# Performance work log

Hardware: AMD Instinct MI355X
Metric: run time of the kernel (lower is better)

## Reference

```python
import jax, jax.numpy as jnp
import numpy as np
import math

B, S, E = 2, 2048, 1024
NH, NKV, HD = 16, 4, 64
GATE_CH = 12

def _rope(x, cos, sin):
    h = x.shape[-1] // 2
    x1, x2 = x[..., :h], x[..., h:]
    return jnp.concatenate((x1 * cos + x2 * sin, x1 * -sin + x2 * cos), axis=-1)

def _rms_norm(x):
    eps = jnp.finfo(x.dtype).eps
    return x * jax.lax.rsqrt(jnp.mean(x * x, axis=-1, keepdims=True) + eps)

def setup_inputs() -> dict:
    key = jax.random.key(0)
    ks = jax.random.split(key, 9)
    x = jax.random.normal(ks[0], (B, S, E), dtype=jnp.float32)
    ve = jax.random.normal(ks[1], (B, S, NKV * HD), dtype=jnp.float32)
    t = jnp.arange(S, dtype=jnp.float32)[:, None]
    inv_freq = 1.0 / (10000.0 ** (jnp.arange(0, HD // 2, dtype=jnp.float32) / (HD // 2)))
    ang = t * inv_freq[None, :]
    cos = jnp.cos(ang)[None, :, None, :]  # (1,S,1,HD//2)
    sin = jnp.sin(ang)[None, :, None, :]
    attn_mask = jnp.tril(jnp.ones((S, S), dtype=bool))[None, None]  # causal (1,1,S,S)
    sc = 0.02
    Wq = jax.random.normal(ks[2], (NH * HD, E), dtype=jnp.float32) * sc
    Wk = jax.random.normal(ks[3], (NKV * HD, E), dtype=jnp.float32) * sc
    Wv = jax.random.normal(ks[4], (NKV * HD, E), dtype=jnp.float32) * sc
    Wproj = jax.random.normal(ks[5], (E, E), dtype=jnp.float32) * sc
    Wgate = jax.random.normal(ks[6], (NKV, GATE_CH), dtype=jnp.float32) * sc
    return {"x": x, "ve": ve, "cos": cos, "sin": sin, "attn_mask": attn_mask,
            "Wq": Wq, "Wk": Wk, "Wv": Wv, "Wproj": Wproj, "Wgate": Wgate}

def reference(x, ve, cos, sin, attn_mask, Wq, Wk, Wv, Wproj, Wgate):
    b, s, _ = x.shape
    q = (x @ Wq.T).reshape(b, s, NH, HD)
    k = (x @ Wk.T).reshape(b, s, NKV, HD)
    v = (x @ Wv.T).reshape(b, s, NKV, HD)
    # value-embedding gating
    gate = 3.0 * jax.nn.sigmoid(x[..., :GATE_CH] @ Wgate.T)  # (b,s,NKV)
    v = v + gate[..., None] * ve.reshape(b, s, NKV, HD)
    # RoPE + QK-RMSNorm
    q = _rms_norm(_rope(q, cos, sin)) * 1.2
    k = _rms_norm(_rope(k, cos, sin)) * 1.2
    # GQA: repeat KV heads
    rep = NH // NKV
    k = jnp.repeat(k, rep, axis=2)
    v = jnp.repeat(v, rep, axis=2)
    q = q.transpose(0, 2, 1, 3)  # (b,h,s,d)
    k = k.transpose(0, 2, 1, 3)
    v = v.transpose(0, 2, 1, 3)
    scores = jnp.einsum('bhqd,bhkd->bhqk', q, k) / math.sqrt(HD)
    scores = jnp.where(attn_mask, scores, jnp.finfo(scores.dtype).min)
    attn = jax.nn.softmax(scores, axis=-1)
    y = jnp.einsum('bhqk,bhkd->bhqd', attn, v)
    y = y.transpose(0, 2, 1, 3).reshape(b, s, NH * HD)
    return y @ Wproj.T
```

## Files before the change

### kernel.cpp

```cpp
#include <hip/hip_runtime.h>
#include <hip/hip_bf16.h>
#include <math.h>

typedef short bf16x8 __attribute__((ext_vector_type(8)));
typedef float f32x4 __attribute__((ext_vector_type(4)));

#define LROW 72

__device__ __forceinline__ unsigned short f2bf(float f) {
  union { float f; unsigned int u; } v; v.f = f;
  unsigned int u = v.u;
  unsigned int r = (u + 0x7fffu + ((u >> 16) & 1u)) >> 16;
  return (unsigned short)r;
}
__device__ __forceinline__ float bf2f(unsigned short u) {
  return __uint_as_float((unsigned)u << 16);
}

#if __has_builtin(__builtin_amdgcn_global_load_lds)
#define HAVE_GLD 1
__device__ __forceinline__ void gld16(const void* g, void* l) {
  __builtin_amdgcn_global_load_lds(
      (const __attribute__((address_space(1))) unsigned int*)g,
      (__attribute__((address_space(3))) unsigned int*)l, 16, 0, 0);
}
#else
#define HAVE_GLD 0
#endif

__global__ __launch_bounds__(256) void cvt_all_kernel(const float* __restrict__ x,
                                                      const float* __restrict__ Wq,
                                                      const float* __restrict__ Wk,
                                                      const float* __restrict__ Wv,
                                                      const float* __restrict__ Wproj,
                                                      unsigned short* __restrict__ xb,
                                                      unsigned short* __restrict__ wqkv,
                                                      unsigned short* __restrict__ wpj) {
  int blk = blockIdx.x;
  const float* src;
  unsigned short* dst;
  if (blk < 4096)      { src = x + (size_t)blk * 1024;            dst = xb + (size_t)blk * 1024; }
  else if (blk < 5120) { src = Wq + (size_t)(blk - 4096) * 1024;  dst = wqkv + (size_t)(blk - 4096) * 1024; }
  else if (blk < 5376) { src = Wk + (size_t)(blk - 5120) * 1024;  dst = wqkv + (size_t)(blk - 4096) * 1024; }
  else if (blk < 5632) { src = Wv + (size_t)(blk - 5376) * 1024;  dst = wqkv + (size_t)(blk - 4096) * 1024; }
  else                 { src = Wproj + (size_t)(blk - 5632) * 1024; dst = wpj + (size_t)(blk - 5632) * 1024; }
  int i = threadIdx.x;
  float4 v = ((const float4*)src)[i];
  ushort4 o;
  o.x = f2bf(v.x); o.y = f2bf(v.y); o.z = f2bf(v.z); o.w = f2bf(v.w);
  ((ushort4*)dst)[i] = o;
}

__global__ __launch_bounds__(256) void gemm128_kernel(const unsigned short* __restrict__ A,
                                                      const unsigned short* __restrict__ B,
                                                      float* __restrict__ C, int M, int N, int K) {
  __shared__ unsigned short As[128 * 64];
  __shared__ unsigned short Bs[128 * 64];
  int tid = threadIdx.x;
  int wave = tid >> 6, lane = tid & 63, l15 = lane & 15, quad = lane >> 4;
  int wm = (wave >> 1) * 64, wn = (wave & 1) * 64;
  int n0 = blockIdx.x * 128, m0 = blockIdx.y * 128;
  f32x4 acc[4][4];
#pragma unroll
  for (int i = 0; i < 4; i++)
#pragma unroll
    for (int j = 0; j < 4; j++) acc[i][j] = (f32x4){0.f, 0.f, 0.f, 0.f};
  int srow = lane >> 3;
  int scol = ((lane & 7) ^ srow) * 8;
  for (int k0 = 0; k0 < K; k0 += 64) {
    __syncthreads();
#if HAVE_GLD
#pragma unroll
    for (int i = 0; i < 4; i++) {
      int row = wave * 32 + i * 8;
      gld16(A + (size_t)(m0 + row + srow) * K + k0 + scol, As + row * 64 + lane * 8);
      gld16(B + (size_t)(n0 + row + srow) * K + k0 + scol, Bs + row * 64 + lane * 8);
    }
#else
#pragma unroll
    for (int i = 0; i < 4; i++) {
      int row = wave * 32 + i * 8;
      *(float4*)(As + row * 64 + lane * 8) = *(const float4*)(A + (size_t)(m0 + row + srow) * K + k0 + scol);
      *(float4*)(Bs + row * 64 + lane * 8) = *(const float4*)(B + (size_t)(n0 + row + srow) * K + k0 + scol);
    }
#endif
    __syncthreads();
#pragma unroll
    for (int s = 0; s < 2; s++) {
      bf16x8 af[4], bf[4];
#pragma unroll
      for (int i = 0; i < 4; i++)
        af[i] = *(const bf16x8*)(As + (wm + i * 16 + l15) * 64 + (((s * 4 + quad) ^ (l15 & 7)) * 8));
#pragma unroll
      for (int j = 0; j < 4; j++)
        bf[j] = *(const bf16x8*)(Bs + (wn + j * 16 + l15) * 64 + (((s * 4 + quad) ^ (l15 & 7)) * 8));
#pragma unroll
      for (int i = 0; i < 4; i++)
#pragma unroll
        for (int j = 0; j < 4; j++)
          acc[i][j] = __builtin_amdgcn_mfma_f32_16x16x32_bf16(af[i], bf[j], acc[i][j], 0, 0, 0);
    }
  }
#pragma unroll
  for (int i = 0; i < 4; i++)
#pragma unroll
    for (int j = 0; j < 4; j++)
#pragma unroll
      for (int r = 0; r < 4; r++)
        C[(size_t)(m0 + wm + i * 16 + quad * 4 + r) * N + n0 + wn + j * 16 + l15] = acc[i][j][r];
}

__global__ __launch_bounds__(256) void gemm_qkv_kernel(const unsigned short* __restrict__ A,
                                                       const unsigned short* __restrict__ B,
                                                       const float* __restrict__ ve,
                                                       const float* __restrict__ cosb,
                                                       const float* __restrict__ sinb,
                                                       const float* __restrict__ wgate,
                                                       unsigned short* __restrict__ Q,
                                                       unsigned short* __restrict__ Kd,
                                                       unsigned short* __restrict__ Vt) {
  __shared__ unsigned short As[128 * 64];
  __shared__ unsigned short Bs[128 * 64];
  __shared__ float gLDS[256];
  const int K = 1024;
  int tid = threadIdx.x;
  int wave = tid >> 6, lane = tid & 63, l15 = lane & 15, quad = lane >> 4;
  int wm = (wave >> 1) * 64, wn = (wave & 1) * 64;
  int n0 = blockIdx.x * 128, m0 = blockIdx.y * 128;
  if (n0 >= 1280) {
    int rl = tid & 127, khl2 = tid >> 7;
    int kh = ((n0 >> 6) - 20) + khl2;
    float dot = 0.f;
#pragma unroll
    for (int jj = 0; jj < 12; jj++)
      dot += bf2f(A[(size_t)(m0 + rl) * 1024 + jj]) * wgate[kh * 12 + jj];
    gLDS[khl2 * 128 + rl] = 3.0f / (1.0f + __expf(-dot));
  }
  f32x4 acc[4][4];
#pragma unroll
  for (int i = 0; i < 4; i++)
#pragma unroll
    for (int j = 0; j < 4; j++) acc[i][j] = (f32x4){0.f, 0.f, 0.f, 0.f};
  int srow = lane >> 3;
  int scol = ((lane & 7) ^ srow) * 8;
  for (int k0 = 0; k0 < K; k0 += 64) {
    __syncthreads();
#if HAVE_GLD
#pragma unroll
    for (int i = 0; i < 4; i++) {
      int row = wave * 32 + i * 8;
      gld16(A + (size_t)(m0 + row + srow) * K + k0 + scol, As + row * 64 + lane * 8);
      gld16(B + (size_t)(n0 + row + srow) * K + k0 + scol, Bs + row * 64 + lane * 8);
    }
#else
#pragma unroll
    for (int i = 0; i < 4; i++) {
      int row = wave * 32 + i * 8;
      *(float4*)(As + row * 64 + lane * 8) = *(const float4*)(A + (size_t)(m0 + row + srow) * K + k0 + scol);
      *(float4*)(Bs + row * 64 + lane * 8) = *(const float4*)(B + (size_t)(n0 + row + srow) * K + k0 + scol);
    }
#endif
    __syncthreads();
#pragma unroll
    for (int s = 0; s < 2; s++) {
      bf16x8 af[4], bf[4];
#pragma unroll
      for (int i = 0; i < 4; i++)
        af[i] = *(const bf16x8*)(As + (wm + i * 16 + l15) * 64 + (((s * 4 + quad) ^ (l15 & 7)) * 8));
#pragma unroll
      for (int j = 0; j < 4; j++)
        bf[j] = *(const bf16x8*)(Bs + (wn + j * 16 + l15) * 64 + (((s * 4 + quad) ^ (l15 & 7)) * 8));
#pragma unroll
      for (int i = 0; i < 4; i++)
#pragma unroll
        for (int j = 0; j < 4; j++)
          acc[i][j] = __builtin_amdgcn_mfma_f32_16x16x32_bf16(af[i], bf[j], acc[i][j], 0, 0, 0);
    }
  }
  int hs = (n0 + wn) >> 6;
  if (hs < 20) {
    bool isq = hs < 16;
    float postscale = isq ? 0.216404256f : 1.2f;
#pragma unroll
    for (int i = 0; i < 4; i++) {
#pragma unroll
      for (int r = 0; r < 4; r++) {
        int row = m0 + wm + i * 16 + quad * 4 + r;
        int s = row & 2047, b = row >> 11;
        float c0 = cosb[s * 32 + l15],      s0 = sinb[s * 32 + l15];
        float c1 = cosb[s * 32 + 16 + l15], s1 = sinb[s * 32 + 16 + l15];
        float v0 = acc[i][0][r], v1 = acc[i][1][r], v2 = acc[i][2][r], v3 = acc[i][3][r];
        float n0v = fmaf(v0, c0,  v2 * s0);
        float n1v = fmaf(v1, c1,  v3 * s1);
        float n2v = fmaf(v2, c0, -v0 * s0);
        float n3v = fmaf(v3, c1, -v1 * s1);
        float ss = (n0v * n0v + n1v * n1v) + (n2v * n2v + n3v * n3v);
        ss += __shfl_xor(ss, 1, 64); ss += __shfl_xor(ss, 2, 64);
        ss += __shfl_xor(ss, 4, 64); ss += __shfl_xor(ss, 8, 64);
        float sc = rsqrtf(ss * (1.0f / 64.0f) + 1.1920929e-07f) * postscale;
        unsigned short* dp = isq ? Q + ((size_t)(b * 16 + hs) * 2048 + s) * 64
                                 : Kd + ((size_t)(b * 4 + hs - 16) * 2048 + s) * 64;
        dp[l15]      = f2bf(n0v * sc);
        dp[16 + l15] = f2bf(n1v * sc);
        dp[32 + l15] = f2bf(n2v * sc);
        dp[48 + l15] = f2bf(n3v * sc);
      }
    }
  } else {
    int khl = wave & 1;
    int kh = hs - 20;
#pragma unroll
    for (int i = 0; i < 4; i++) {
#pragma unroll
      for (int r = 0; r < 4; r++) {
        int rl = wm + i * 16 + quad * 4 + r;
        int row = m0 + rl, s = row & 2047, b = row >> 11;
        float g = gLDS[khl * 128 + rl];
        const float* vep = ve + (size_t)row * 256 + kh * 64;
        unsigned short* vp = Vt + ((size_t)(b * 4 + kh) * 64) * 2048 + s;
#pragma unroll
        for (int j = 0; j < 4; j++) {
          float vv = fmaf(g, vep[j * 16 + l15], acc[i][j][r]);
          vp[(size_t)(j * 16 + l15) * 2048] = f2bf(vv);
        }
      }
    }
  }
}

__global__ __launch_bounds__(256) void flash_kernel(const unsigned short* __restrict__ Q,
                                                    const unsigned short* __restrict__ K,
                                                    const unsigned short* __restrict__ Vt,
                                                    unsigned short* __restrict__ accP,
                                                    float* __restrict__ lP) {
  __shared__ unsigned short Ks[64 * LROW];
  __shared__ unsigned short Vs[64 * LROW];
  __shared__ unsigned short Ps[4 * 16 * LROW];
  int pair = blockIdx.x, h = blockIdx.y, bc = blockIdx.z;
  int b = bc >> 2, c = bc & 3;
  int hb = b * 16 + h;
  int kh = h >> 2;
  int tid = threadIdx.x, wave = tid >> 6, lane = tid & 63, l15 = lane & 15, quad = lane >> 4;
  const unsigned short* Kg = K + (size_t)(b * 4 + kh) * 2048 * 64;
  const unsigned short* Vg = Vt + (size_t)(b * 4 + kh) * 64 * 2048;
  unsigned short* Pw = Ps + wave * 16 * LROW;
  int row0 = tid >> 3, col8 = (tid & 7) * 8;

#pragma unroll
  for (int half = 0; half < 2; half++) {
    int qt = (half == 0) ? pair : 31 - pair;
    int c0t = ((qt + 1) * c) >> 2;
    int c1t = ((qt + 1) * (c + 1)) >> 2;
    int q0 = qt * 64;
    const unsigned short* Qp = Q + (((size_t)hb * 2048) + q0 + wave * 16 + l15) * 64;
    bf16x8 qf0 = *(const bf16x8*)(Qp + quad * 8);
    bf16x8 qf1 = *(const bf16x8*)(Qp + 32 + quad * 8);
    f32x4 acc[4];
#pragma unroll
    for (int i = 0; i < 4; i++) acc[i] = (f32x4){0.f, 0.f, 0.f, 0.f};
    float l_lane = 0.f;

    if (c1t > c0t) {
      int kf = c0t * 64;
      float4 pk0 = *(const float4*)(Kg + (size_t)(kf + row0) * 64 + col8);
      float4 pk1 = *(const float4*)(Kg + (size_t)(kf + row0 + 32) * 64 + col8);
      float4 pv0 = *(const float4*)(Vg + (size_t)row0 * 2048 + kf + col8);
      float4 pv1 = *(const float4*)(Vg + (size_t)(row0 + 32) * 2048 + kf + col8);

      for (int kt = c0t; kt < c1t; kt++) {
        int k0 = kt * 64;
        __syncthreads();
        *(float4*)(Ks + row0 * LROW + col8) = pk0;
        *(float4*)(Ks + (row0 + 32) * LROW + col8) = pk1;
        *(float4*)(Vs + row0 * LROW + col8) = pv0;
        *(float4*)(Vs + (row0 + 32) * LROW + col8) = pv1;
        if (kt + 1 < c1t) {
          int kn = k0 + 64;
          pk0 = *(const float4*)(Kg + (size_t)(kn + row0) * 64 + col8);
          pk1 = *(const float4*)(Kg + (size_t)(kn + row0 + 32) * 64 + col8);
          pv0 = *(const float4*)(Vg + (size_t)row0 * 2048 + kn + col8);
          pv1 = *(const float4*)(Vg + (size_t)(row0 + 32) * 2048 + kn + col8);
        }
        __syncthreads();

        f32x4 sv[4];
#pragma unroll
        for (int mt = 0; mt < 4; mt++) {
          sv[mt] = (f32x4){0.f, 0.f, 0.f, 0.f};
          bf16x8 k0f = *(const bf16x8*)(Ks + (mt * 16 + l15) * LROW + quad * 8);
          sv[mt] = __builtin_amdgcn_mfma_f32_16x16x32_bf16(k0f, qf0, sv[mt], 0, 0, 0);
          bf16x8 k1f = *(const bf16x8*)(Ks + (mt * 16 + l15) * LROW + 32 + quad * 8);
          sv[mt] = __builtin_amdgcn_mfma_f32_16x16x32_bf16(k1f, qf1, sv[mt], 0, 0, 0);
        }
        if (kt == qt) {
          int qg = q0 + wave * 16 + l15;
#pragma unroll
          for (int mt = 0; mt < 4; mt++) {
            int kg = k0 + mt * 16 + quad * 4;
#pragma unroll
            for (int r = 0; r < 4; r++)
              if (kg + r > qg) sv[mt][r] = -1e30f;
          }
        }
#pragma unroll
        for (int mt = 0; mt < 4; mt++) {
          float p0 = __builtin_amdgcn_exp2f(sv[mt][0]);
          float p1 = __builtin_amdgcn_exp2f(sv[mt][1]);
          float p2 = __builtin_amdgcn_exp2f(sv[mt][2]);
          float p3 = __builtin_amdgcn_exp2f(sv[mt][3]);
          l_lane += (p0 + p1) + (p2 + p3);
          unsigned int lo = __builtin_amdgcn_perm(__float_as_uint(p1), __float_as_uint(p0), 0x07060302u);
          unsigned int hi = __builtin_amdgcn_perm(__float_as_uint(p3), __float_as_uint(p2), 0x07060302u);
          *(uint2*)(Pw + l15 * LROW + mt * 16 + quad * 4) = make_uint2(lo, hi);
        }
#pragma unroll
        for (int step = 0; step < 2; step++) {
          bf16x8 pa = *(const bf16x8*)(Pw + l15 * LROW + step * 32 + quad * 8);
#pragma unroll
          for (int nt = 0; nt < 4; nt++) {
            bf16x8 vb = *(const bf16x8*)(Vs + (nt * 16 + l15) * LROW + step * 32 + quad * 8);
            acc[nt] = __builtin_amdgcn_mfma_f32_16x16x32_bf16(pa, vb, acc[nt], 0, 0, 0);
          }
        }
      }
    }
    l_lane += __shfl_xor(l_lane, 16, 64);
    l_lane += __shfl_xor(l_lane, 32, 64);

    size_t slot = (size_t)(c * 32 + hb) * 2048 + q0 + wave * 16;
    if (lane < 16) lP[slot + l15] = l_lane;
    unsigned short* aP = accP + slot * 64;
#pragma unroll
    for (int r = 0; r < 4; r++)
#pragma unroll
      for (int nt = 0; nt < 4; nt++)
        aP[(size_t)(quad * 4 + r) * 64 + nt * 16 + l15] = f2bf(acc[nt][r]);
  }
}

__global__ __launch_bounds__(256) void merge_kernel(const unsigned short* __restrict__ accP,
                                                    const float* __restrict__ lP,
                                                    unsigned short* __restrict__ Y) {
  int t = blockIdx.x * 256 + threadIdx.x;
  int d4 = (t & 15) * 4;
  int q  = (t >> 4) & 2047;
  int hb = t >> 15;
  const size_t CSTR = (size_t)32 * 2048 * 64;
  size_t pi = ((size_t)hb * 2048 + q) * 64 + d4;
  float y0 = 0.f, y1 = 0.f, y2 = 0.f, y3 = 0.f, l = 0.f;
#pragma unroll
  for (int c = 0; c < 4; c++) {
    ushort4 a = *(const ushort4*)(accP + pi + c * CSTR);
    y0 += bf2f(a.x); y1 += bf2f(a.y); y2 += bf2f(a.z); y3 += bf2f(a.w);
    l += lP[c * 65536 + hb * 2048 + q];
  }
  float inv = 1.f / l;
  ushort4 o;
  o.x = f2bf(y0 * inv); o.y = f2bf(y1 * inv); o.z = f2bf(y2 * inv); o.w = f2bf(y3 * inv);
  int b = hb >> 4, hh = hb & 15;
  *(ushort4*)(Y + ((size_t)(b * 2048 + q) * 1024) + hh * 64 + d4) = o;
}

extern "C" void kernel_launch(void* const* d_in, const int* in_sizes, int n_in,
                              void* d_out, int out_size, void* d_ws, size_t ws_size,
                              hipStream_t stream) {
  const float* x     = (const float*)d_in[0];
  const float* ve    = (const float*)d_in[1];
  const float* cosb  = (const float*)d_in[2];
  const float* sinb  = (const float*)d_in[3];
  const float* Wq    = (const float*)d_in[5];
  const float* Wk    = (const float*)d_in[6];
  const float* Wv    = (const float*)d_in[7];
  const float* Wproj = (const float*)d_in[8];
  const float* Wgate = (const float*)d_in[9];
  float* out = (float*)d_out;
  char* ws = (char*)d_ws;

  size_t o = 0;
  unsigned short* xb   = (unsigned short*)(ws + o); o += (size_t)4096 * 1024 * 2;
  unsigned short* wqkv = (unsigned short*)(ws + o); o += (size_t)1536 * 1024 * 2;
  unsigned short* wpj  = (unsigned short*)(ws + o); o += (size_t)1024 * 1024 * 2;
  unsigned short* Qb   = (unsigned short*)(ws + o); o += (size_t)2 * 16 * 2048 * 64 * 2;
  unsigned short* Kb   = (unsigned short*)(ws + o); o += (size_t)2 * 4 * 2048 * 64 * 2;
  unsigned short* Vb   = (unsigned short*)(ws + o); o += (size_t)2 * 4 * 2048 * 64 * 2;
  unsigned short* Yb   = (unsigned short*)(ws + o); o += (size_t)4096 * 1024 * 2;
  unsigned short* accP = (unsigned short*)(ws + o); o += (size_t)4 * 32 * 2048 * 64 * 2;
  float*          lP   = (float*)(ws + o);          o += (size_t)4 * 32 * 2048 * 4;

  hipLaunchKernelGGL(cvt_all_kernel, dim3(6656), dim3(256), 0, stream,
                     x, Wq, Wk, Wv, Wproj, xb, wqkv, wpj);
  hipLaunchKernelGGL(gemm_qkv_kernel, dim3(12, 32), dim3(256), 0, stream,
                     xb, wqkv, ve, cosb, sinb, Wgate, Qb, Kb, Vb);
  hipLaunchKernelGGL(flash_kernel, dim3(16, 16, 8), dim3(256), 0, stream, Qb, Kb, Vb, accP, lP);
  hipLaunchKernelGGL(merge_kernel, dim3(4096), dim3(256), 0, stream, accP, lP, Yb);
  hipLaunchKernelGGL(gemm128_kernel, dim3(8, 32), dim3(256), 0, stream, Yb, wpj, out, 4096, 1024, 1024);
}
```

Before: 200.3 us.

## Share KV tiles across GQA heads in flash kernel with double-buffered async loads

Each flash block now handles all four query heads that share one KV head, so every K/V tile loaded into LDS is reused four times. The grid drops from 16 heads to 4 KV heads, and the split-K factor rises from 4 to 6 to keep the block count up. K/V are double-buffered and loaded with global_load_lds into an XOR-swizzled unpadded layout, and the fragments are held in registers. In exchange the kernel uses more registers (four accumulator sets and Q fragments), and the merge kernel reads more partial sums.

```diff
diff --git a/kernel.cpp b/kernel.cpp
--- a/kernel.cpp
+++ b/kernel.cpp
@@ -6,6 +6,7 @@
 typedef float f32x4 __attribute__((ext_vector_type(4)));
 
 #define LROW 72
+#define NSPLIT 6
 
 __device__ __forceinline__ unsigned short f2bf(float f) {
   union { float f; unsigned int u; } v; v.f = f;
@@ -233,108 +234,136 @@
                                                     const unsigned short* __restrict__ Vt,
                                                     unsigned short* __restrict__ accP,
                                                     float* __restrict__ lP) {
-  __shared__ unsigned short Ks[64 * LROW];
-  __shared__ unsigned short Vs[64 * LROW];
+  __shared__ unsigned short Ks[2][64 * 64];
+  __shared__ unsigned short Vs[2][64 * 64];
   __shared__ unsigned short Ps[4 * 16 * LROW];
-  int pair = blockIdx.x, h = blockIdx.y, bc = blockIdx.z;
-  int b = bc >> 2, c = bc & 3;
-  int hb = b * 16 + h;
-  int kh = h >> 2;
+  int pair = blockIdx.x, kh = blockIdx.y, bc = blockIdx.z;
+  int b = bc / NSPLIT, c = bc % NSPLIT;
   int tid = threadIdx.x, wave = tid >> 6, lane = tid & 63, l15 = lane & 15, quad = lane >> 4;
   const unsigned short* Kg = K + (size_t)(b * 4 + kh) * 2048 * 64;
   const unsigned short* Vg = Vt + (size_t)(b * 4 + kh) * 64 * 2048;
   unsigned short* Pw = Ps + wave * 16 * LROW;
-  int row0 = tid >> 3, col8 = (tid & 7) * 8;
+  int srow = lane >> 3;
+  int scol = ((lane & 7) ^ srow) * 8;
 
 #pragma unroll
   for (int half = 0; half < 2; half++) {
     int qt = (half == 0) ? pair : 31 - pair;
-    int c0t = ((qt + 1) * c) >> 2;
-    int c1t = ((qt + 1) * (c + 1)) >> 2;
+    int c0t = ((qt + 1) * c) / NSPLIT;
+    int c1t = ((qt + 1) * (c + 1)) / NSPLIT;
     int q0 = qt * 64;
-    const unsigned short* Qp = Q + (((size_t)hb * 2048) + q0 + wave * 16 + l15) * 64;
-    bf16x8 qf0 = *(const bf16x8*)(Qp + quad * 8);
-    bf16x8 qf1 = *(const bf16x8*)(Qp + 32 + quad * 8);
-    f32x4 acc[4];
-#pragma unroll
-    for (int i = 0; i < 4; i++) acc[i] = (f32x4){0.f, 0.f, 0.f, 0.f};
-    float l_lane = 0.f;
+    bf16x8 qf[4][2];
+#pragma unroll
+    for (int h = 0; h < 4; h++) {
+      const unsigned short* Qp =
+          Q + (((size_t)(b * 16 + kh * 4 + h) * 2048) + q0 + wave * 16 + l15) * 64;
+      qf[h][0] = *(const bf16x8*)(Qp + quad * 8);
+      qf[h][1] = *(const bf16x8*)(Qp + 32 + quad * 8);
+    }
+    f32x4 acc[4][4];
+#pragma unroll
+    for (int h = 0; h < 4; h++)
+#pragma unroll
+      for (int i = 0; i < 4; i++) acc[h][i] = (f32x4){0.f, 0.f, 0.f, 0.f};
+    float l_lane[4] = {0.f, 0.f, 0.f, 0.f};
 
     if (c1t > c0t) {
-      int kf = c0t * 64;
-      float4 pk0 = *(const float4*)(Kg + (size_t)(kf + row0) * 64 + col8);
-      float4 pk1 = *(const float4*)(Kg + (size_t)(kf + row0 + 32) * 64 + col8);
-      float4 pv0 = *(const float4*)(Vg + (size_t)row0 * 2048 + kf + col8);
-      float4 pv1 = *(const float4*)(Vg + (size_t)(row0 + 32) * 2048 + kf + col8);
-
-      for (int kt = c0t; kt < c1t; kt++) {
-        int k0 = kt * 64;
-        __syncthreads();
-        *(float4*)(Ks + row0 * LROW + col8) = pk0;
-        *(float4*)(Ks + (row0 + 32) * LROW + col8) = pk1;
-        *(float4*)(Vs + row0 * LROW + col8) = pv0;
-        *(float4*)(Vs + (row0 + 32) * LROW + col8) = pv1;
-        if (kt + 1 < c1t) {
-          int kn = k0 + 64;
-          pk0 = *(const float4*)(Kg + (size_t)(kn + row0) * 64 + col8);
-          pk1 = *(const float4*)(Kg + (size_t)(kn + row0 + 32) * 64 + col8);
-          pv0 = *(const float4*)(Vg + (size_t)row0 * 2048 + kn + col8);
-          pv1 = *(const float4*)(Vg + (size_t)(row0 + 32) * 2048 + kn + col8);
-        }
-        __syncthreads();
-
-        f32x4 sv[4];
-#pragma unroll
-        for (int mt = 0; mt < 4; mt++) {
-          sv[mt] = (f32x4){0.f, 0.f, 0.f, 0.f};
-          bf16x8 k0f = *(const bf16x8*)(Ks + (mt * 16 + l15) * LROW + quad * 8);
-          sv[mt] = __builtin_amdgcn_mfma_f32_16x16x32_bf16(k0f, qf0, sv[mt], 0, 0, 0);
-          bf16x8 k1f = *(const bf16x8*)(Ks + (mt * 16 + l15) * LROW + 32 + quad * 8);
-          sv[mt] = __builtin_amdgcn_mfma_f32_16x16x32_bf16(k1f, qf1, sv[mt], 0, 0, 0);
-        }
-        if (kt == qt) {
-          int qg = q0 + wave * 16 + l15;
-#pragma unroll
-          for (int mt = 0; mt < 4; mt++) {
-            int kg = k0 + mt * 16 + quad * 4;
-#pragma unroll
-            for (int r = 0; r < 4; r++)
-              if (kg + r > qg) sv[mt][r] = -1e30f;
-          }
-        }
-#pragma unroll
-        for (int mt = 0; mt < 4; mt++) {
-          float p0 = __builtin_amdgcn_exp2f(sv[mt][0]);
-          float p1 = __builtin_amdgcn_exp2f(sv[mt][1]);
-          float p2 = __builtin_amdgcn_exp2f(sv[mt][2]);
-          float p3 = __builtin_amdgcn_exp2f(sv[mt][3]);
-          l_lane += (p0 + p1) + (p2 + p3);
-          unsigned int lo = __builtin_amdgcn_perm(__float_as_uint(p1), __float_as_uint(p0), 0x07060302u);
-          unsigned int hi = __builtin_amdgcn_perm(__float_as_uint(p3), __float_as_uint(p2), 0x07060302u);
-          *(uint2*)(Pw + l15 * LROW + mt * 16 + quad * 4) = make_uint2(lo, hi);
-        }
-#pragma unroll
-        for (int step = 0; step < 2; step++) {
-          bf16x8 pa = *(const bf16x8*)(Pw + l15 * LROW + step * 32 + quad * 8);
-#pragma unroll
-          for (int nt = 0; nt < 4; nt++) {
-            bf16x8 vb = *(const bf16x8*)(Vs + (nt * 16 + l15) * LROW + step * 32 + quad * 8);
-            acc[nt] = __builtin_amdgcn_mfma_f32_16x16x32_bf16(pa, vb, acc[nt], 0, 0, 0);
-          }
+      {
+        int k0 = c0t * 64;
+#pragma unroll
+        for (int j = 0; j < 2; j++) {
+          int row = wave * 16 + j * 8;
+#if HAVE_GLD
+          gld16(Kg + (size_t)(k0 + row + srow) * 64 + scol, Ks[0] + row * 64 + lane * 8);
+          gld16(Vg + (size_t)(row + srow) * 2048 + k0 + scol, Vs[0] + row * 64 + lane * 8);
+#else
+          *(float4*)(Ks[0] + row * 64 + lane * 8) = *(const float4*)(Kg + (size_t)(k0 + row + srow) * 64 + scol);
+          *(float4*)(Vs[0] + row * 64 + lane * 8) = *(const float4*)(Vg + (size_t)(row + srow) * 2048 + k0 + scol);
+#endif
         }
       }
-    }
-    l_lane += __shfl_xor(l_lane, 16, 64);
-    l_lane += __shfl_xor(l_lane, 32, 64);
-
-    size_t slot = (size_t)(c * 32 + hb) * 2048 + q0 + wave * 16;
-    if (lane < 16) lP[slot + l15] = l_lane;
-    unsigned short* aP = accP + slot * 64;
-#pragma unroll
-    for (int r = 0; r < 4; r++)
-#pragma unroll
-      for (int nt = 0; nt < 4; nt++)
-        aP[(size_t)(quad * 4 + r) * 64 + nt * 16 + l15] = f2bf(acc[nt][r]);
+      for (int kt = c0t; kt < c1t; kt++) {
+        int buf = (kt - c0t) & 1;
+        __syncthreads();
+        if (kt + 1 < c1t) {
+          int kn = (kt + 1) * 64;
+#pragma unroll
+          for (int j = 0; j < 2; j++) {
+            int row = wave * 16 + j * 8;
+#if HAVE_GLD
+            gld16(Kg + (size_t)(kn + row + srow) * 64 + scol, Ks[buf ^ 1] + row * 64 + lane * 8);
+            gld16(Vg + (size_t)(row + srow) * 2048 + kn + scol, Vs[buf ^ 1] + row * 64 + lane * 8);
+#else
+            *(float4*)(Ks[buf ^ 1] + row * 64 + lane * 8) = *(const float4*)(Kg + (size_t)(kn + row + srow) * 64 + scol);
+            *(float4*)(Vs[buf ^ 1] + row * 64 + lane * 8) = *(const float4*)(Vg + (size_t)(row + srow) * 2048 + kn + scol);
+#endif
+          }
+        }
+        bf16x8 kf[4][2], vf[4][2];
+#pragma unroll
+        for (int mt = 0; mt < 4; mt++) {
+#pragma unroll
+          for (int s2 = 0; s2 < 2; s2++) {
+            kf[mt][s2] = *(const bf16x8*)(Ks[buf] + (mt * 16 + l15) * 64 + (((s2 * 4 + quad) ^ (l15 & 7)) * 8));
+            vf[mt][s2] = *(const bf16x8*)(Vs[buf] + (mt * 16 + l15) * 64 + (((s2 * 4 + quad) ^ (l15 & 7)) * 8));
+          }
+        }
+        int k0 = kt * 64;
+        bool diag = (kt == qt);
+        int qg = q0 + wave * 16 + l15;
+#pragma unroll
+        for (int h = 0; h < 4; h++) {
+          f32x4 sv[4];
+#pragma unroll
+          for (int mt = 0; mt < 4; mt++) {
+            sv[mt] = (f32x4){0.f, 0.f, 0.f, 0.f};
+            sv[mt] = __builtin_amdgcn_mfma_f32_16x16x32_bf16(kf[mt][0], qf[h][0], sv[mt], 0, 0, 0);
+            sv[mt] = __builtin_amdgcn_mfma_f32_16x16x32_bf16(kf[mt][1], qf[h][1], sv[mt], 0, 0, 0);
+          }
+          if (diag) {
+#pragma unroll
+            for (int mt = 0; mt < 4; mt++) {
+              int kg = k0 + mt * 16 + quad * 4;
+#pragma unroll
+              for (int r = 0; r < 4; r++)
+                if (kg + r > qg) sv[mt][r] = -1e30f;
+            }
+          }
+#pragma unroll
+          for (int mt = 0; mt < 4; mt++) {
+            float p0 = __builtin_amdgcn_exp2f(sv[mt][0]);
+            float p1 = __builtin_amdgcn_exp2f(sv[mt][1]);
+            float p2 = __builtin_amdgcn_exp2f(sv[mt][2]);
+            float p3 = __builtin_amdgcn_exp2f(sv[mt][3]);
+            l_lane[h] += (p0 + p1) + (p2 + p3);
+            unsigned int lo = __builtin_amdgcn_perm(__float_as_uint(p1), __float_as_uint(p0), 0x07060302u);
+            unsigned int hi = __builtin_amdgcn_perm(__float_as_uint(p3), __float_as_uint(p2), 0x07060302u);
+            *(uint2*)(Pw + l15 * LROW + mt * 16 + quad * 4) = make_uint2(lo, hi);
+          }
+#pragma unroll
+          for (int step = 0; step < 2; step++) {
+            bf16x8 pa = *(const bf16x8*)(Pw + l15 * LROW + step * 32 + quad * 8);
+#pragma unroll
+            for (int nt = 0; nt < 4; nt++)
+              acc[h][nt] = __builtin_amdgcn_mfma_f32_16x16x32_bf16(pa, vf[nt][step], acc[h][nt], 0, 0, 0);
+          }
+        }
+      }
+    }
+#pragma unroll
+    for (int h = 0; h < 4; h++) {
+      float l = l_lane[h];
+      l += __shfl_xor(l, 16, 64);
+      l += __shfl_xor(l, 32, 64);
+      size_t slot = (size_t)(c * 32 + b * 16 + kh * 4 + h) * 2048 + q0 + wave * 16;
+      if (lane < 16) lP[slot + l15] = l;
+      unsigned short* aP = accP + slot * 64;
+#pragma unroll
+      for (int r = 0; r < 4; r++)
+#pragma unroll
+        for (int nt = 0; nt < 4; nt++)
+          aP[(size_t)(quad * 4 + r) * 64 + nt * 16 + l15] = f2bf(acc[h][nt][r]);
+    }
   }
 }
 
@@ -349,7 +378,7 @@
   size_t pi = ((size_t)hb * 2048 + q) * 64 + d4;
   float y0 = 0.f, y1 = 0.f, y2 = 0.f, y3 = 0.f, l = 0.f;
 #pragma unroll
-  for (int c = 0; c < 4; c++) {
+  for (int c = 0; c < NSPLIT; c++) {
     ushort4 a = *(const ushort4*)(accP + pi + c * CSTR);
     y0 += bf2f(a.x); y1 += bf2f(a.y); y2 += bf2f(a.z); y3 += bf2f(a.w);
     l += lP[c * 65536 + hb * 2048 + q];
@@ -384,14 +413,15 @@
   unsigned short* Kb   = (unsigned short*)(ws + o); o += (size_t)2 * 4 * 2048 * 64 * 2;
   unsigned short* Vb   = (unsigned short*)(ws + o); o += (size_t)2 * 4 * 2048 * 64 * 2;
   unsigned short* Yb   = (unsigned short*)(ws + o); o += (size_t)4096 * 1024 * 2;
-  unsigned short* accP = (unsigned short*)(ws + o); o += (size_t)4 * 32 * 2048 * 64 * 2;
-  float*          lP   = (float*)(ws + o);          o += (size_t)4 * 32 * 2048 * 4;
+  unsigned short* accP = (unsigned short*)(ws + o); o += (size_t)NSPLIT * 32 * 2048 * 64 * 2;
+  float*          lP   = (float*)(ws + o);          o += (size_t)NSPLIT * 32 * 2048 * 4;
 
   hipLaunchKernelGGL(cvt_all_kernel, dim3(6656), dim3(256), 0, stream,
                      x, Wq, Wk, Wv, Wproj, xb, wqkv, wpj);
   hipLaunchKernelGGL(gemm_qkv_kernel, dim3(12, 32), dim3(256), 0, stream,
                      xb, wqkv, ve, cosb, sinb, Wgate, Qb, Kb, Vb);
-  hipLaunchKernelGGL(flash_kernel, dim3(16, 16, 8), dim3(256), 0, stream, Qb, Kb, Vb, accP, lP);
+  hipLaunchKernelGGL(flash_kernel, dim3(16, 4, 2 * NSPLIT), dim3(256), 0, stream,
+                     Qb, Kb, Vb, accP, lP);
   hipLaunchKernelGGL(merge_kernel, dim3(4096), dim3(256), 0, stream, accP, lP, Yb);
   hipLaunchKernelGGL(gemm128_kernel, dim3(8, 32), dim3(256), 0, stream, Yb, wpj, out, 4096, 1024, 1024);
 }
```

New measurement: 224.2 us. 1.12x slower.

## Fuse split-K merge into projection GEMM, halve KV splits, double-buffer flash K/V

Applied to the files above, without the earlier changes.

The separate merge kernel is removed. The output-projection GEMM now reads the two partial attention accumulators and their row sums directly, normalizes them, and writes the bf16 A tile into LDS. The flash kernel splits the KV range into 2 chunks instead of 4, which halves the partial-buffer traffic. K/V tiles are now staged through double-buffered swizzled LDS using direct global-to-LDS loads, replacing register prefetch and padded rows. In exchange, the flash grid has fewer blocks, so parallelism is lower. The merge work is also recomputed once per N-tile of the projection GEMM.

```diff
diff --git a/kernel.cpp b/kernel.cpp
--- a/kernel.cpp
+++ b/kernel.cpp
@@ -51,65 +51,6 @@
   ((ushort4*)dst)[i] = o;
 }
 
-__global__ __launch_bounds__(256) void gemm128_kernel(const unsigned short* __restrict__ A,
-                                                      const unsigned short* __restrict__ B,
-                                                      float* __restrict__ C, int M, int N, int K) {
-  __shared__ unsigned short As[128 * 64];
-  __shared__ unsigned short Bs[128 * 64];
-  int tid = threadIdx.x;
-  int wave = tid >> 6, lane = tid & 63, l15 = lane & 15, quad = lane >> 4;
-  int wm = (wave >> 1) * 64, wn = (wave & 1) * 64;
-  int n0 = blockIdx.x * 128, m0 = blockIdx.y * 128;
-  f32x4 acc[4][4];
-#pragma unroll
-  for (int i = 0; i < 4; i++)
-#pragma unroll
-    for (int j = 0; j < 4; j++) acc[i][j] = (f32x4){0.f, 0.f, 0.f, 0.f};
-  int srow = lane >> 3;
-  int scol = ((lane & 7) ^ srow) * 8;
-  for (int k0 = 0; k0 < K; k0 += 64) {
-    __syncthreads();
-#if HAVE_GLD
-#pragma unroll
-    for (int i = 0; i < 4; i++) {
-      int row = wave * 32 + i * 8;
-      gld16(A + (size_t)(m0 + row + srow) * K + k0 + scol, As + row * 64 + lane * 8);
-      gld16(B + (size_t)(n0 + row + srow) * K + k0 + scol, Bs + row * 64 + lane * 8);
-    }
-#else
-#pragma unroll
-    for (int i = 0; i < 4; i++) {
-      int row = wave * 32 + i * 8;
-      *(float4*)(As + row * 64 + lane * 8) = *(const float4*)(A + (size_t)(m0 + row + srow) * K + k0 + scol);
-      *(float4*)(Bs + row * 64 + lane * 8) = *(const float4*)(B + (size_t)(n0 + row + srow) * K + k0 + scol);
-    }
-#endif
-    __syncthreads();
-#pragma unroll
-    for (int s = 0; s < 2; s++) {
-      bf16x8 af[4], bf[4];
-#pragma unroll
-      for (int i = 0; i < 4; i++)
-        af[i] = *(const bf16x8*)(As + (wm + i * 16 + l15) * 64 + (((s * 4 + quad) ^ (l15 & 7)) * 8));
-#pragma unroll
-      for (int j = 0; j < 4; j++)
-        bf[j] = *(const bf16x8*)(Bs + (wn + j * 16 + l15) * 64 + (((s * 4 + quad) ^ (l15 & 7)) * 8));
-#pragma unroll
-      for (int i = 0; i < 4; i++)
-#pragma unroll
-        for (int j = 0; j < 4; j++)
-          acc[i][j] = __builtin_amdgcn_mfma_f32_16x16x32_bf16(af[i], bf[j], acc[i][j], 0, 0, 0);
-    }
-  }
-#pragma unroll
-  for (int i = 0; i < 4; i++)
-#pragma unroll
-    for (int j = 0; j < 4; j++)
-#pragma unroll
-      for (int r = 0; r < 4; r++)
-        C[(size_t)(m0 + wm + i * 16 + quad * 4 + r) * N + n0 + wn + j * 16 + l15] = acc[i][j][r];
-}
-
 __global__ __launch_bounds__(256) void gemm_qkv_kernel(const unsigned short* __restrict__ A,
                                                        const unsigned short* __restrict__ B,
                                                        const float* __restrict__ ve,
@@ -233,24 +174,25 @@
                                                     const unsigned short* __restrict__ Vt,
                                                     unsigned short* __restrict__ accP,
                                                     float* __restrict__ lP) {
-  __shared__ unsigned short Ks[64 * LROW];
-  __shared__ unsigned short Vs[64 * LROW];
+  __shared__ unsigned short Ks[2][64 * 64];
+  __shared__ unsigned short Vs[2][64 * 64];
   __shared__ unsigned short Ps[4 * 16 * LROW];
   int pair = blockIdx.x, h = blockIdx.y, bc = blockIdx.z;
-  int b = bc >> 2, c = bc & 3;
+  int b = bc >> 1, c = bc & 1;
   int hb = b * 16 + h;
   int kh = h >> 2;
   int tid = threadIdx.x, wave = tid >> 6, lane = tid & 63, l15 = lane & 15, quad = lane >> 4;
   const unsigned short* Kg = K + (size_t)(b * 4 + kh) * 2048 * 64;
   const unsigned short* Vg = Vt + (size_t)(b * 4 + kh) * 64 * 2048;
   unsigned short* Pw = Ps + wave * 16 * LROW;
-  int row0 = tid >> 3, col8 = (tid & 7) * 8;
+  int srow = lane >> 3;
+  int scol = ((lane & 7) ^ srow) * 8;
 
 #pragma unroll
   for (int half = 0; half < 2; half++) {
     int qt = (half == 0) ? pair : 31 - pair;
-    int c0t = ((qt + 1) * c) >> 2;
-    int c1t = ((qt + 1) * (c + 1)) >> 2;
+    int c0t = (c == 0) ? 0 : (qt + 2) >> 1;
+    int c1t = (c == 0) ? ((qt + 2) >> 1) : qt + 1;
     int q0 = qt * 64;
     const unsigned short* Qp = Q + (((size_t)hb * 2048) + q0 + wave * 16 + l15) * 64;
     bf16x8 qf0 = *(const bf16x8*)(Qp + quad * 8);
@@ -261,35 +203,45 @@
     float l_lane = 0.f;
 
     if (c1t > c0t) {
-      int kf = c0t * 64;
-      float4 pk0 = *(const float4*)(Kg + (size_t)(kf + row0) * 64 + col8);
-      float4 pk1 = *(const float4*)(Kg + (size_t)(kf + row0 + 32) * 64 + col8);
-      float4 pv0 = *(const float4*)(Vg + (size_t)row0 * 2048 + kf + col8);
-      float4 pv1 = *(const float4*)(Vg + (size_t)(row0 + 32) * 2048 + kf + col8);
-
+      {
+        int k0 = c0t * 64;
+#pragma unroll
+        for (int j = 0; j < 2; j++) {
+          int row = wave * 16 + j * 8;
+#if HAVE_GLD
+          gld16(Kg + (size_t)(k0 + row + srow) * 64 + scol, Ks[0] + row * 64 + lane * 8);
+          gld16(Vg + (size_t)(row + srow) * 2048 + k0 + scol, Vs[0] + row * 64 + lane * 8);
+#else
+          *(float4*)(Ks[0] + row * 64 + lane * 8) = *(const float4*)(Kg + (size_t)(k0 + row + srow) * 64 + scol);
+          *(float4*)(Vs[0] + row * 64 + lane * 8) = *(const float4*)(Vg + (size_t)(row + srow) * 2048 + k0 + scol);
+#endif
+        }
+      }
       for (int kt = c0t; kt < c1t; kt++) {
+        int buf = (kt - c0t) & 1;
+        __syncthreads();
+        if (kt + 1 < c1t) {
+          int kn = (kt + 1) * 64;
+#pragma unroll
+          for (int j = 0; j < 2; j++) {
+            int row = wave * 16 + j * 8;
+#if HAVE_GLD
+            gld16(Kg + (size_t)(kn + row + srow) * 64 + scol, Ks[buf ^ 1] + row * 64 + lane * 8);
+            gld16(Vg + (size_t)(row + srow) * 2048 + kn + scol, Vs[buf ^ 1] + row * 64 + lane * 8);
+#else
+            *(float4*)(Ks[buf ^ 1] + row * 64 + lane * 8) = *(const float4*)(Kg + (size_t)(kn + row + srow) * 64 + scol);
+            *(float4*)(Vs[buf ^ 1] + row * 64 + lane * 8) = *(const float4*)(Vg + (size_t)(row + srow) * 2048 + kn + scol);
+#endif
+          }
+        }
         int k0 = kt * 64;
-        __syncthreads();
-        *(float4*)(Ks + row0 * LROW + col8) = pk0;
-        *(float4*)(Ks + (row0 + 32) * LROW + col8) = pk1;
-        *(float4*)(Vs + row0 * LROW + col8) = pv0;
-        *(float4*)(Vs + (row0 + 32) * LROW + col8) = pv1;
-        if (kt + 1 < c1t) {
-          int kn = k0 + 64;
-          pk0 = *(const float4*)(Kg + (size_t)(kn + row0) * 64 + col8);
-          pk1 = *(const float4*)(Kg + (size_t)(kn + row0 + 32) * 64 + col8);
-          pv0 = *(const float4*)(Vg + (size_t)row0 * 2048 + kn + col8);
-          pv1 = *(const float4*)(Vg + (size_t)(row0 + 32) * 2048 + kn + col8);
-        }
-        __syncthreads();
-
         f32x4 sv[4];
 #pragma unroll
         for (int mt = 0; mt < 4; mt++) {
           sv[mt] = (f32x4){0.f, 0.f, 0.f, 0.f};
-          bf16x8 k0f = *(const bf16x8*)(Ks + (mt * 16 + l15) * LROW + quad * 8);
+          bf16x8 k0f = *(const bf16x8*)(Ks[buf] + (mt * 16 + l15) * 64 + ((quad ^ (l15 & 7)) * 8));
           sv[mt] = __builtin_amdgcn_mfma_f32_16x16x32_bf16(k0f, qf0, sv[mt], 0, 0, 0);
-          bf16x8 k1f = *(const bf16x8*)(Ks + (mt * 16 + l15) * LROW + 32 + quad * 8);
+          bf16x8 k1f = *(const bf16x8*)(Ks[buf] + (mt * 16 + l15) * 64 + (((4 + quad) ^ (l15 & 7)) * 8));
           sv[mt] = __builtin_amdgcn_mfma_f32_16x16x32_bf16(k1f, qf1, sv[mt], 0, 0, 0);
         }
         if (kt == qt) {
@@ -318,7 +270,7 @@
           bf16x8 pa = *(const bf16x8*)(Pw + l15 * LROW + step * 32 + quad * 8);
 #pragma unroll
           for (int nt = 0; nt < 4; nt++) {
-            bf16x8 vb = *(const bf16x8*)(Vs + (nt * 16 + l15) * LROW + step * 32 + quad * 8);
+            bf16x8 vb = *(const bf16x8*)(Vs[buf] + (nt * 16 + l15) * 64 + (((step * 4 + quad) ^ (l15 & 7)) * 8));
             acc[nt] = __builtin_amdgcn_mfma_f32_16x16x32_bf16(pa, vb, acc[nt], 0, 0, 0);
           }
         }
@@ -338,27 +290,77 @@
   }
 }
 
-__global__ __launch_bounds__(256) void merge_kernel(const unsigned short* __restrict__ accP,
-                                                    const float* __restrict__ lP,
-                                                    unsigned short* __restrict__ Y) {
-  int t = blockIdx.x * 256 + threadIdx.x;
-  int d4 = (t & 15) * 4;
-  int q  = (t >> 4) & 2047;
-  int hb = t >> 15;
+__global__ __launch_bounds__(256) void gemm_proj_kernel(const unsigned short* __restrict__ accP,
+                                                        const float* __restrict__ lP,
+                                                        const unsigned short* __restrict__ B,
+                                                        float* __restrict__ C) {
+  __shared__ unsigned short As[128 * 64];
+  __shared__ unsigned short Bs[128 * 64];
+  const int K = 1024, N = 1024;
   const size_t CSTR = (size_t)32 * 2048 * 64;
-  size_t pi = ((size_t)hb * 2048 + q) * 64 + d4;
-  float y0 = 0.f, y1 = 0.f, y2 = 0.f, y3 = 0.f, l = 0.f;
-#pragma unroll
-  for (int c = 0; c < 4; c++) {
-    ushort4 a = *(const ushort4*)(accP + pi + c * CSTR);
-    y0 += bf2f(a.x); y1 += bf2f(a.y); y2 += bf2f(a.z); y3 += bf2f(a.w);
-    l += lP[c * 65536 + hb * 2048 + q];
-  }
-  float inv = 1.f / l;
-  ushort4 o;
-  o.x = f2bf(y0 * inv); o.y = f2bf(y1 * inv); o.z = f2bf(y2 * inv); o.w = f2bf(y3 * inv);
-  int b = hb >> 4, hh = hb & 15;
-  *(ushort4*)(Y + ((size_t)(b * 2048 + q) * 1024) + hh * 64 + d4) = o;
+  int tid = threadIdx.x;
+  int wave = tid >> 6, lane = tid & 63, l15 = lane & 15, quad = lane >> 4;
+  int wm = (wave >> 1) * 64, wn = (wave & 1) * 64;
+  int n0 = blockIdx.x * 128, m0 = blockIdx.y * 128;
+  f32x4 acc[4][4];
+#pragma unroll
+  for (int i = 0; i < 4; i++)
+#pragma unroll
+    for (int j = 0; j < 4; j++) acc[i][j] = (f32x4){0.f, 0.f, 0.f, 0.f};
+  int srow = lane >> 3;
+  int scol = ((lane & 7) ^ srow) * 8;
+  for (int k0 = 0; k0 < K; k0 += 64) {
+    int h = k0 >> 6;
+    __syncthreads();
+#pragma unroll
+    for (int i = 0; i < 4; i++) {
+      int row = wave * 32 + i * 8;
+#if HAVE_GLD
+      gld16(B + (size_t)(n0 + row + srow) * K + k0 + scol, Bs + row * 64 + lane * 8);
+#else
+      *(float4*)(Bs + row * 64 + lane * 8) = *(const float4*)(B + (size_t)(n0 + row + srow) * K + k0 + scol);
+#endif
+      int gr = m0 + row + srow;
+      int q = gr & 2047, bb = gr >> 11;
+      size_t base = ((size_t)((bb * 16 + h) * 2048) + q) * 64 + scol;
+      uint4 a0 = *(const uint4*)(accP + base);
+      uint4 a1 = *(const uint4*)(accP + base + CSTR);
+      float inv = 1.f / (lP[(bb * 16 + h) * 2048 + q] + lP[65536 + (bb * 16 + h) * 2048 + q]);
+      unsigned int w[4];
+#pragma unroll
+      for (int e = 0; e < 4; e++) {
+        unsigned int u0 = ((const unsigned int*)&a0)[e];
+        unsigned int u1 = ((const unsigned int*)&a1)[e];
+        float lo = (__uint_as_float(u0 << 16) + __uint_as_float(u1 << 16)) * inv;
+        float hi = (__uint_as_float(u0 & 0xffff0000u) + __uint_as_float(u1 & 0xffff0000u)) * inv;
+        w[e] = ((unsigned int)f2bf(lo)) | (((unsigned int)f2bf(hi)) << 16);
+      }
+      *(uint4*)(As + row * 64 + lane * 8) = make_uint4(w[0], w[1], w[2], w[3]);
+    }
+    __syncthreads();
+#pragma unroll
+    for (int s = 0; s < 2; s++) {
+      bf16x8 af[4], bf[4];
+#pragma unroll
+      for (int i = 0; i < 4; i++)
+        af[i] = *(const bf16x8*)(As + (wm + i * 16 + l15) * 64 + (((s * 4 + quad) ^ (l15 & 7)) * 8));
+#pragma unroll
+      for (int j = 0; j < 4; j++)
+        bf[j] = *(const bf16x8*)(Bs + (wn + j * 16 + l15) * 64 + (((s * 4 + quad) ^ (l15 & 7)) * 8));
+#pragma unroll
+      for (int i = 0; i < 4; i++)
+#pragma unroll
+        for (int j = 0; j < 4; j++)
+          acc[i][j] = __builtin_amdgcn_mfma_f32_16x16x32_bf16(af[i], bf[j], acc[i][j], 0, 0, 0);
+    }
+  }
+#pragma unroll
+  for (int i = 0; i < 4; i++)
+#pragma unroll
+    for (int j = 0; j < 4; j++)
+#pragma unroll
+      for (int r = 0; r < 4; r++)
+        C[(size_t)(m0 + wm + i * 16 + quad * 4 + r) * N + n0 + wn + j * 16 + l15] = acc[i][j][r];
 }
 
 extern "C" void kernel_launch(void* const* d_in, const int* in_sizes, int n_in,
@@ -383,15 +385,13 @@
   unsigned short* Qb   = (unsigned short*)(ws + o); o += (size_t)2 * 16 * 2048 * 64 * 2;
   unsigned short* Kb   = (unsigned short*)(ws + o); o += (size_t)2 * 4 * 2048 * 64 * 2;
   unsigned short* Vb   = (unsigned short*)(ws + o); o += (size_t)2 * 4 * 2048 * 64 * 2;
-  unsigned short* Yb   = (unsigned short*)(ws + o); o += (size_t)4096 * 1024 * 2;
-  unsigned short* accP = (unsigned short*)(ws + o); o += (size_t)4 * 32 * 2048 * 64 * 2;
-  float*          lP   = (float*)(ws + o);          o += (size_t)4 * 32 * 2048 * 4;
+  unsigned short* accP = (unsigned short*)(ws + o); o += (size_t)2 * 32 * 2048 * 64 * 2;
+  float*          lP   = (float*)(ws + o);          o += (size_t)2 * 32 * 2048 * 4;
 
   hipLaunchKernelGGL(cvt_all_kernel, dim3(6656), dim3(256), 0, stream,
                      x, Wq, Wk, Wv, Wproj, xb, wqkv, wpj);
   hipLaunchKernelGGL(gemm_qkv_kernel, dim3(12, 32), dim3(256), 0, stream,
                      xb, wqkv, ve, cosb, sinb, Wgate, Qb, Kb, Vb);
-  hipLaunchKernelGGL(flash_kernel, dim3(16, 16, 8), dim3(256), 0, stream, Qb, Kb, Vb, accP, lP);
-  hipLaunchKernelGGL(merge_kernel, dim3(4096), dim3(256), 0, stream, accP, lP, Yb);
-  hipLaunchKernelGGL(gemm128_kernel, dim3(8, 32), dim3(256), 0, stream, Yb, wpj, out, 4096, 1024, 1024);
-}
+  hipLaunchKernelGGL(flash_kernel, dim3(16, 16, 4), dim3(256), 0, stream, Qb, Kb, Vb, accP, lP);
+  hipLaunchKernelGGL(gemm_proj_kernel, dim3(8, 32), dim3(256), 0, stream, accP, lP, wpj, out);
+}
```

New measurement: 211.4 us. +5.6%, slower.

## Halve flash KV split count and XOR-swizzle K/V shared memory tiles

Applied to the files above, without the earlier changes.

Reduces the key-range split of the attention kernel from four chunks to two, so each block processes longer KV ranges and the partial-accumulator workspace and merge reads shrink. K and V tiles in LDS change from padded rows to unpadded 64-wide rows with an XOR chunk swizzle, which is meant to avoid bank conflicts while saving LDS. The cost is half as many flash blocks, which lowers parallelism and may hurt load balance across CUs.

```diff
diff --git a/kernel.cpp b/kernel.cpp
--- a/kernel.cpp
+++ b/kernel.cpp
@@ -6,6 +6,7 @@
 typedef float f32x4 __attribute__((ext_vector_type(4)));
 
 #define LROW 72
+#define NSPLIT 2
 
 __device__ __forceinline__ unsigned short f2bf(float f) {
   union { float f; unsigned int u; } v; v.f = f;
@@ -233,24 +234,26 @@
                                                     const unsigned short* __restrict__ Vt,
                                                     unsigned short* __restrict__ accP,
                                                     float* __restrict__ lP) {
-  __shared__ unsigned short Ks[64 * LROW];
-  __shared__ unsigned short Vs[64 * LROW];
+  __shared__ unsigned short Ks[64 * 64];
+  __shared__ unsigned short Vs[64 * 64];
   __shared__ unsigned short Ps[4 * 16 * LROW];
   int pair = blockIdx.x, h = blockIdx.y, bc = blockIdx.z;
-  int b = bc >> 2, c = bc & 3;
+  int b = bc >> 1, c = bc & 1;
   int hb = b * 16 + h;
   int kh = h >> 2;
   int tid = threadIdx.x, wave = tid >> 6, lane = tid & 63, l15 = lane & 15, quad = lane >> 4;
+  int l7 = l15 & 7;
   const unsigned short* Kg = K + (size_t)(b * 4 + kh) * 2048 * 64;
   const unsigned short* Vg = Vt + (size_t)(b * 4 + kh) * 64 * 2048;
   unsigned short* Pw = Ps + wave * 16 * LROW;
   int row0 = tid >> 3, col8 = (tid & 7) * 8;
+  int dchunk = (((tid & 7) ^ (row0 & 7)) * 8);
 
 #pragma unroll
   for (int half = 0; half < 2; half++) {
     int qt = (half == 0) ? pair : 31 - pair;
-    int c0t = ((qt + 1) * c) >> 2;
-    int c1t = ((qt + 1) * (c + 1)) >> 2;
+    int c0t = (c == 0) ? 0 : (qt + 2) >> 1;
+    int c1t = (c == 0) ? ((qt + 2) >> 1) : qt + 1;
     int q0 = qt * 64;
     const unsigned short* Qp = Q + (((size_t)hb * 2048) + q0 + wave * 16 + l15) * 64;
     bf16x8 qf0 = *(const bf16x8*)(Qp + quad * 8);
@@ -270,10 +273,10 @@
       for (int kt = c0t; kt < c1t; kt++) {
         int k0 = kt * 64;
         __syncthreads();
-        *(float4*)(Ks + row0 * LROW + col8) = pk0;
-        *(float4*)(Ks + (row0 + 32) * LROW + col8) = pk1;
-        *(float4*)(Vs + row0 * LROW + col8) = pv0;
-        *(float4*)(Vs + (row0 + 32) * LROW + col8) = pv1;
+        *(float4*)(Ks + row0 * 64 + dchunk) = pk0;
+        *(float4*)(Ks + (row0 + 32) * 64 + dchunk) = pk1;
+        *(float4*)(Vs + row0 * 64 + dchunk) = pv0;
+        *(float4*)(Vs + (row0 + 32) * 64 + dchunk) = pv1;
         if (kt + 1 < c1t) {
           int kn = k0 + 64;
           pk0 = *(const float4*)(Kg + (size_t)(kn + row0) * 64 + col8);
@@ -287,9 +290,9 @@
 #pragma unroll
         for (int mt = 0; mt < 4; mt++) {
           sv[mt] = (f32x4){0.f, 0.f, 0.f, 0.f};
-          bf16x8 k0f = *(const bf16x8*)(Ks + (mt * 16 + l15) * LROW + quad * 8);
+          bf16x8 k0f = *(const bf16x8*)(Ks + (mt * 16 + l15) * 64 + ((quad ^ l7) * 8));
           sv[mt] = __builtin_amdgcn_mfma_f32_16x16x32_bf16(k0f, qf0, sv[mt], 0, 0, 0);
-          bf16x8 k1f = *(const bf16x8*)(Ks + (mt * 16 + l15) * LROW + 32 + quad * 8);
+          bf16x8 k1f = *(const bf16x8*)(Ks + (mt * 16 + l15) * 64 + (((4 + quad) ^ l7) * 8));
           sv[mt] = __builtin_amdgcn_mfma_f32_16x16x32_bf16(k1f, qf1, sv[mt], 0, 0, 0);
         }
         if (kt == qt) {
@@ -318,7 +321,7 @@
           bf16x8 pa = *(const bf16x8*)(Pw + l15 * LROW + step * 32 + quad * 8);
 #pragma unroll
           for (int nt = 0; nt < 4; nt++) {
-            bf16x8 vb = *(const bf16x8*)(Vs + (nt * 16 + l15) * LROW + step * 32 + quad * 8);
+            bf16x8 vb = *(const bf16x8*)(Vs + (nt * 16 + l15) * 64 + (((step * 4 + quad) ^ l7) * 8));
             acc[nt] = __builtin_amdgcn_mfma_f32_16x16x32_bf16(pa, vb, acc[nt], 0, 0, 0);
           }
         }
@@ -349,7 +352,7 @@
   size_t pi = ((size_t)hb * 2048 + q) * 64 + d4;
   float y0 = 0.f, y1 = 0.f, y2 = 0.f, y3 = 0.f, l = 0.f;
 #pragma unroll
-  for (int c = 0; c < 4; c++) {
+  for (int c = 0; c < NSPLIT; c++) {
     ushort4 a = *(const ushort4*)(accP + pi + c * CSTR);
     y0 += bf2f(a.x); y1 += bf2f(a.y); y2 += bf2f(a.z); y3 += bf2f(a.w);
     l += lP[c * 65536 + hb * 2048 + q];
@@ -384,14 +387,15 @@
   unsigned short* Kb   = (unsigned short*)(ws + o); o += (size_t)2 * 4 * 2048 * 64 * 2;
   unsigned short* Vb   = (unsigned short*)(ws + o); o += (size_t)2 * 4 * 2048 * 64 * 2;
   unsigned short* Yb   = (unsigned short*)(ws + o); o += (size_t)4096 * 1024 * 2;
-  unsigned short* accP = (unsigned short*)(ws + o); o += (size_t)4 * 32 * 2048 * 64 * 2;
-  float*          lP   = (float*)(ws + o);          o += (size_t)4 * 32 * 2048 * 4;
+  unsigned short* accP = (unsigned short*)(ws + o); o += (size_t)NSPLIT * 32 * 2048 * 64 * 2;
+  float*          lP   = (float*)(ws + o);          o += (size_t)NSPLIT * 32 * 2048 * 4;
 
   hipLaunchKernelGGL(cvt_all_kernel, dim3(6656), dim3(256), 0, stream,
                      x, Wq, Wk, Wv, Wproj, xb, wqkv, wpj);
   hipLaunchKernelGGL(gemm_qkv_kernel, dim3(12, 32), dim3(256), 0, stream,
                      xb, wqkv, ve, cosb, sinb, Wgate, Qb, Kb, Vb);
-  hipLaunchKernelGGL(flash_kernel, dim3(16, 16, 8), dim3(256), 0, stream, Qb, Kb, Vb, accP, lP);
+  hipLaunchKernelGGL(flash_kernel, dim3(16, 16, 2 * NSPLIT), dim3(256), 0, stream,
+                     Qb, Kb, Vb, accP, lP);
   hipLaunchKernelGGL(merge_kernel, dim3(4096), dim3(256), 0, stream, accP, lP, Yb);
   hipLaunchKernelGGL(gemm128_kernel, dim3(8, 32), dim3(256), 0, stream, Yb, wpj, out, 4096, 1024, 1024);
 }
```

Measured after the change: 192.4 us. -3.9%, faster.
